# Performance work log

Measured on AMD Instinct MI355X. Metric: run time of the kernel, lower is better.

Reference implementation:

```python
import jax, jax.numpy as jnp
import numpy as np

N_NODES = 100000
N_EDGES = 1600000


def gcn_conv(x, W, b, src, dst, ew, n):
    """PyG GCNConv: x@W, symmetric deg^-1/2 norm with self-loops, scatter-add at dst, +b."""
    loop = jnp.arange(n, dtype=src.dtype)
    s = jnp.concatenate([src, loop])            # sources incl. self-loops
    d = jnp.concatenate([dst, loop])            # targets incl. self-loops
    w = jnp.concatenate([ew, jnp.ones((n,), ew.dtype)])  # self-loop weight = 1
    deg = jax.ops.segment_sum(w, d, num_segments=n)      # weighted in-degree
    dinv = jnp.where(deg > 0, jax.lax.rsqrt(deg), 0.0)
    norm = dinv[s] * w * dinv[d]                # [E+N]
    h = x @ W                                   # [N, F_out]
    msg = h[s] * norm[:, None]                  # gather + per-edge scale
    out = jax.ops.segment_sum(msg, d, num_segments=n)    # scatter-add
    return out + b


def setup_inputs() -> dict:
    key = jax.random.key(0)
    ks = jax.random.split(key, 8)
    in_dim, hid, lat = 128, 128, 64
    x = jax.random.normal(ks[0], (N_NODES, in_dim), jnp.float32)
    edge_index = jax.random.randint(ks[1], (2, N_EDGES), 0, N_NODES, dtype=jnp.int32)
    weights = jax.random.uniform(ks[2], (N_EDGES,), jnp.float32)
    s_in = 1.0 / np.sqrt(in_dim)
    s_h = 1.0 / np.sqrt(hid)
    return {
        "x": x,
        "edge_index": edge_index,
        "weights": weights,
        "W1": jax.random.normal(ks[3], (in_dim, hid), jnp.float32) * s_in,
        "b1": jnp.zeros((hid,), jnp.float32),
        "W2": jax.random.normal(ks[4], (hid, hid), jnp.float32) * s_h,
        "b2": jnp.zeros((hid,), jnp.float32),
        "W_mu": jax.random.normal(ks[5], (hid, lat), jnp.float32) * s_h,
        "b_mu": jnp.zeros((lat,), jnp.float32),
        "W_lv": jax.random.normal(ks[6], (hid, lat), jnp.float32) * s_h,
        "b_lv": jnp.zeros((lat,), jnp.float32),
    }


def reference(x, edge_index, weights, W1, b1, W2, b2, W_mu, b_mu, W_lv, b_lv):
    n = x.shape[0]
    src, dst = edge_index[0], edge_index[1]
    h = jax.nn.relu(gcn_conv(x, W1, b1, src, dst, weights, n))
    h = gcn_conv(h, W2, b2, src, dst, weights, n)
    g = jnp.mean(h, axis=0, keepdims=True)      # [1, hid] global mean pool
    mu = g @ W_mu + b_mu
    logvar = g @ W_lv + b_lv
    return (mu, logvar)
```

## Files before the change

### kernel.cpp

```cpp
#include <hip/hip_runtime.h>


typedef __bf16 bf16x8 __attribute__((ext_vector_type(8)));
typedef float f32x4 __attribute__((ext_vector_type(4)));
typedef float f32x2 __attribute__((ext_vector_type(2)));
typedef unsigned long long u64;

#define RE   2048
#define BSH  8
#define BCAP 5120
#define NBMX 392

__device__ __forceinline__ float bf2f(unsigned short u){
  return __uint_as_float(((unsigned)u) << 16);
}
__device__ __forceinline__ unsigned short f2bf(float f){
  unsigned u = __float_as_uint(f);
  u += 0x7fffu + ((u >> 16) & 1u);
  return (unsigned short)(u >> 16);
}
__device__ __forceinline__ __bf16 us2bf(unsigned short u){
  __bf16 b; __builtin_memcpy(&b, &u, 2); return b;
}
__device__ __forceinline__ float ldf(const void* p, int i, int isf32){
  return isf32 ? ((const float*)p)[i] : bf2f(((const unsigned short*)p)[i]);
}
__device__ __forceinline__ void fma8f8(float* acc, float n, uint2 h){
  f32x2 p0 = __builtin_amdgcn_cvt_pk_f32_fp8((int)h.x, false);
  f32x2 p1 = __builtin_amdgcn_cvt_pk_f32_fp8((int)h.x, true);
  f32x2 p2 = __builtin_amdgcn_cvt_pk_f32_fp8((int)h.y, false);
  f32x2 p3 = __builtin_amdgcn_cvt_pk_f32_fp8((int)h.y, true);
  acc[0] = fmaf(n, p0[0], acc[0]);
  acc[1] = fmaf(n, p0[1], acc[1]);
  acc[2] = fmaf(n, p1[0], acc[2]);
  acc[3] = fmaf(n, p1[1], acc[3]);
  acc[4] = fmaf(n, p2[0], acc[4]);
  acc[5] = fmaf(n, p2[1], acc[5]);
  acc[6] = fmaf(n, p3[0], acc[6]);
  acc[7] = fmaf(n, p3[1], acc[7]);
}

__device__ __forceinline__ void scanBuckets(int* __restrict__ cnt, int* __restrict__ sm,
    int* __restrict__ hrow, int* __restrict__ rrow, int NB, int tid){
  const int K = (NBMX + 255) / 256;
  int c0 = tid * K;
  int loc = 0;
  #pragma unroll
  for (int i = 0; i < K; ++i){
    int j = c0 + i;
    if (j < NB) loc += cnt[j];
  }
  sm[tid] = loc;
  __syncthreads();
  for (int off = 1; off < 256; off <<= 1){
    int tmp = (tid >= off) ? sm[tid - off] : 0;
    __syncthreads();
    sm[tid] += tmp;
    __syncthreads();
  }
  int running = sm[tid] - loc;
  #pragma unroll
  for (int i = 0; i < K; ++i){
    int j = c0 + i;
    if (j < NB){
      int old = cnt[j];
      hrow[j] = old;
      rrow[j] = running;
      cnt[j] = running;
      running += old;
    }
  }
}

__global__ void k_init(const unsigned* __restrict__ xw, int* __restrict__ flag,
                       const void* __restrict__ W1, unsigned short* __restrict__ W1T,
                       float* __restrict__ v){
  __shared__ int s[256];
  int t = threadIdx.x;
  int cnt = 0;
  for (int k = t; k < 4096; k += 256){
    unsigned lo = xw[k] & 0xFFFFu;
    int e = (int)((lo >> 7) & 0xFFu);
    if ((e >= 100 && e <= 141) || (lo & 0x7FFFu) == 0) cnt++;
  }
  s[t] = cnt;
  __syncthreads();
  for (int off = 128; off > 0; off >>= 1){
    if (t < off) s[t] += s[t + off];
    __syncthreads();
  }
  int isf32 = (s[0] < 2458) ? 1 : 0;
  if (blockIdx.x == 0){
    if (t == 0) *flag = isf32;
    if (t < 128) v[t] = 0.0f;
  }
  int gid = blockIdx.x * 256 + t;
  int k = gid & 127, n = gid >> 7;
  W1T[gid] = isf32 ? f2bf(((const float*)W1)[k * 128 + n])
                   : ((const unsigned short*)W1)[k * 128 + n];
}

__global__ void __launch_bounds__(256) k_bin1(const int* __restrict__ src,
    const int* __restrict__ dst, const void* __restrict__ w,
    u64* __restrict__ stagD, u64* __restrict__ stagS,
    int* __restrict__ histD, int* __restrict__ roffD,
    int* __restrict__ histS, int* __restrict__ roffS,
    int E, int NB, const int* __restrict__ flagp){
  __shared__ int cntD[NBMX];
  __shared__ int cntS[NBMX];
  __shared__ u64 stag[RE];
  __shared__ int sm[256];
  int tid = threadIdx.x;
  int r = blockIdx.x;
  for (int i = tid; i < NB; i += 256){ cntD[i] = 0; cntS[i] = 0; }
  __syncthreads();
  int isf32 = *flagp;
  int e0 = r * RE;
  int en = E - e0; if (en > RE) en = RE;
  u64 rec[8];
  #pragma unroll
  for (int k = 0; k < 8; ++k){
    int o = k * 256 + tid;
    rec[k] = ~0ull;
    if (o < en){
      int idx = e0 + o;
      int s_ = src[idx], d_ = dst[idx];
      float wf = ldf(w, idx, isf32);
      int wq = (int)(wf * 32768.0f + 0.5f);
      if (wq > 32767) wq = 32767;
      rec[k] = ((u64)(unsigned)d_ << 32) | ((u64)(unsigned)s_ << 15) | (unsigned)wq;
      atomicAdd(&cntD[d_ >> BSH], 1);
      atomicAdd(&cntS[s_ >> BSH], 1);
    }
  }
  __syncthreads();
  scanBuckets(cntD, sm, histD + (size_t)r * NB, roffD + (size_t)r * NB, NB, tid);
  __syncthreads();
  #pragma unroll
  for (int k = 0; k < 8; ++k){
    if (rec[k] != ~0ull){
      int p = atomicAdd(&cntD[(int)(rec[k] >> 32) >> BSH], 1);
      stag[p] = rec[k];
    }
  }
  __syncthreads();
  u64* opD = stagD + (size_t)r * RE;
  for (int i = tid; i < en; i += 256) opD[i] = stag[i];
  __syncthreads();
  scanBuckets(cntS, sm, histS + (size_t)r * NB, roffS + (size_t)r * NB, NB, tid);
  __syncthreads();
  #pragma unroll
  for (int k = 0; k < 8; ++k){
    if (rec[k] != ~0ull){
      int d_ = (int)(rec[k] >> 32);
      int s_ = (int)((rec[k] >> 15) & 0x1FFFFu);
      unsigned wq = (unsigned)(rec[k] & 32767u);
      u64 rs = ((u64)(unsigned)s_ << 32) | ((u64)(unsigned)d_ << 15) | wq;
      int p = atomicAdd(&cntS[s_ >> BSH], 1);
      stag[p] = rs;
    }
  }
  __syncthreads();
  u64* opS = stagS + (size_t)r * RE;
  for (int i = tid; i < en; i += 256) opS[i] = stag[i];
}

__global__ void __launch_bounds__(256) k_transp(const int* __restrict__ A,
    const int* __restrict__ B, int* __restrict__ AT, int* __restrict__ BT,
    int NR, int NB){
  __shared__ int ta[32][33];
  __shared__ int tb[32][33];
  int bx = (int)blockIdx.x * 32;
  int by = (int)blockIdx.y * 32;
  int tx = threadIdx.x & 31, ty = threadIdx.x >> 5;
  for (int yy = ty; yy < 32; yy += 8){
    int r = by + yy, b = bx + tx;
    int v1 = 0, v2 = 0;
    if (r < NR && b < NB){
      v1 = A[(size_t)r * NB + b];
      v2 = B[(size_t)r * NB + b];
    }
    ta[yy][tx] = v1; tb[yy][tx] = v2;
  }
  __syncthreads();
  for (int yy = ty; yy < 32; yy += 8){
    int b = bx + yy, r = by + tx;
    if (b < NB && r < NR){
      AT[(size_t)b * NR + r] = ta[tx][yy];
      BT[(size_t)b * NR + r] = tb[tx][yy];
    }
  }
}

__global__ void __launch_bounds__(512) k_pass2a(const u64* __restrict__ staging,
    const int* __restrict__ histT, const int* __restrict__ roffT,
    float* __restrict__ dinv, int* __restrict__ cnt, int* __restrict__ rowptr,
    int* __restrict__ bsum, int NR, int N){
  __shared__ unsigned cd[256];
  __shared__ int sm[512];
  int b = blockIdx.x, tid = threadIdx.x;
  int lo = b << BSH;
  int nn = N - lo; if (nn > 256) nn = 256;
  if (tid < 256) cd[tid] = 0u;
  __syncthreads();
  const int* hrow = histT + (size_t)b * NR;
  const int* rrow = roffT + (size_t)b * NR;
  for (int r = tid; r < NR; r += 512){
    int len = hrow[r];
    if (len == 0) continue;
    const u64* rp = staging + (size_t)r * RE + rrow[r];
    for (int k = 0; k < len; ++k){
      u64 rec = rp[k];
      int dl = (int)(rec >> 32) - lo;
      atomicAdd(&cd[dl], (1u << 20) | (unsigned)((rec & 32767u) >> 2));
    }
  }
  __syncthreads();
  int val = 0;
  if (tid < nn){
    unsigned p = cd[tid];
    dinv[lo + tid] = rsqrtf(1.0f + (float)(p & 0xFFFFFu) * (1.0f / 8192.0f));
    cnt[lo + tid] = (int)(p >> 20);
    val = (int)(p >> 20);
  }
  sm[tid] = val;
  __syncthreads();
  for (int off = 1; off < 512; off <<= 1){
    int tmp = (tid >= off) ? sm[tid - off] : 0;
    __syncthreads();
    sm[tid] += tmp;
    __syncthreads();
  }
  if (tid < nn) rowptr[lo + tid] = sm[tid] - val;
  if (tid == 511) bsum[b] = sm[511];
}

__global__ void k_scanB(const int* __restrict__ bsum, int* __restrict__ boffs, int NB){
  __shared__ int s[512];
  int t = threadIdx.x;
  int val = (t < NB) ? bsum[t] : 0;
  s[t] = val;
  __syncthreads();
  for (int off = 1; off < 512; off <<= 1){
    int tmp = (t >= off) ? s[t - off] : 0;
    __syncthreads();
    s[t] += tmp;
    __syncthreads();
  }
  boffs[t] = s[t] - val;
}

__global__ void k_scanC(int* __restrict__ rowptr, const int* __restrict__ boffs, int N){
  int i = blockIdx.x * 256 + threadIdx.x;
  if (i >= N) return;
  rowptr[i] = rowptr[i] + boffs[blockIdx.x];
}

__global__ void __launch_bounds__(512) k_pass2S(const u64* __restrict__ stagS,
    const int* __restrict__ histST, const int* __restrict__ roffST,
    const float* __restrict__ dinv, float* __restrict__ S, int NR, int N){
  __shared__ float SL[256];
  int b = blockIdx.x, tid = threadIdx.x;
  int lo = b << BSH;
  int nn = N - lo; if (nn > 256) nn = 256;
  if (tid < 256) SL[tid] = 0.0f;
  __syncthreads();
  const int* hrow = histST + (size_t)b * NR;
  const int* rrow = roffST + (size_t)b * NR;
  for (int r = tid; r < NR; r += 512){
    int len = hrow[r];
    if (len == 0) continue;
    const u64* rp = stagS + (size_t)r * RE + rrow[r];
    for (int k = 0; k < len; ++k){
      u64 rec = rp[k];
      int s_ = (int)(rec >> 32);
      int d_ = (int)((rec >> 15) & 0x1FFFFu);
      float wqf = (float)(rec & 32767u) * (1.0f / 32768.0f);
      atomicAdd(&SL[s_ - lo], wqf * dinv[d_]);
    }
  }
  __syncthreads();
  if (tid < nn) S[lo + tid] = SL[tid];
}

__global__ void __launch_bounds__(512) k_pass2b(const u64* __restrict__ staging,
    const int* __restrict__ histT, const int* __restrict__ roffT,
    const float* __restrict__ dinv, const int* __restrict__ rowptr,
    const int* __restrict__ cnt, unsigned* __restrict__ edges, int NR, int N){
  __shared__ unsigned recs[BCAP];
  __shared__ int cur[256];
  __shared__ int sb[2];
  int b = blockIdx.x, tid = threadIdx.x;
  int lo = b << BSH;
  int nn = N - lo; if (nn > 256) nn = 256;
  if (tid == 0){
    int base = rowptr[lo];
    sb[0] = base;
    sb[1] = rowptr[lo + nn - 1] + cnt[lo + nn - 1] - base;
  }
  __syncthreads();
  int base = sb[0], tot = sb[1];
  if (tot > BCAP) tot = BCAP;
  if (tid < nn) cur[tid] = rowptr[lo + tid] - base;
  __syncthreads();
  const int* hrow = histT + (size_t)b * NR;
  const int* rrow = roffT + (size_t)b * NR;
  for (int r = tid; r < NR; r += 512){
    int len = hrow[r];
    if (len == 0) continue;
    const u64* rp = staging + (size_t)r * RE + rrow[r];
    for (int k = 0; k < len; ++k){
      u64 rec = rp[k];
      int d_ = (int)(rec >> 32);
      int s_ = (int)((rec >> 15) & 0x1FFFFu);
      int wq = (int)(rec & 32767u);
      float nrm = dinv[s_] * ((float)wq * (1.0f / 32768.0f)) * dinv[d_];
      int nq = (int)(nrm * 32768.0f + 0.5f);
      if (nq > 32767) nq = 32767;
      int p = atomicAdd(&cur[d_ - lo], 1);
      if (p < BCAP) recs[p] = ((unsigned)s_ << 15) | (unsigned)nq;
    }
  }
  __syncthreads();
  unsigned* op = edges + base;
  for (int i = tid; i < tot; i += 512) op[i] = recs[i];
}

__global__ void k_cfacm(const float* __restrict__ S, const float* __restrict__ dinv,
                        const int* __restrict__ rowptr, const int* __restrict__ cnt,
                        float2* __restrict__ dc, int2* __restrict__ rc,
                        unsigned* __restrict__ edges, int E, int N){
  if (blockIdx.x == 0 && threadIdx.x < 16) edges[E + threadIdx.x] = 0u;
  int i = blockIdx.x * 256 + threadIdx.x;
  if (i >= N) return;
  float di = dinv[i];
  dc[i] = make_float2(di * di, di * di + di * S[i]);
  rc[i] = make_int2(rowptr[i], cnt[i]);
}

__global__ void __launch_bounds__(256) k_gemm(const void* __restrict__ xv,
                                              const __bf16* __restrict__ wt,
                                              unsigned char* __restrict__ H, int N,
                                              const int* __restrict__ flagp){
  int wave = (blockIdx.x * blockDim.x + threadIdx.x) >> 6;
  int lane = threadIdx.x & 63;
  int row16 = wave << 4;
  if (row16 >= N) return;
  int isf32 = *flagp;
  int m = lane & 15, q = lane >> 4;
  bf16x8 a0, a1, a2, a3;
  if (isf32){
    const float* ap = (const float*)xv + (size_t)(row16 + m) * 128 + q * 8;
    #pragma unroll
    for (int j = 0; j < 8; ++j){
      a0[j] = us2bf(f2bf(ap[j +  0]));
      a1[j] = us2bf(f2bf(ap[j + 32]));
      a2[j] = us2bf(f2bf(ap[j + 64]));
      a3[j] = us2bf(f2bf(ap[j + 96]));
    }
  } else {
    const __bf16* ap = (const __bf16*)xv + (size_t)(row16 + m) * 128 + q * 8;
    a0 = *(const bf16x8*)(ap +  0);
    a1 = *(const bf16x8*)(ap + 32);
    a2 = *(const bf16x8*)(ap + 64);
    a3 = *(const bf16x8*)(ap + 96);
  }
  for (int nt = 0; nt < 8; ++nt){
    const __bf16* bp = wt + (size_t)(nt * 16 + m) * 128 + q * 8;
    bf16x8 b0 = *(const bf16x8*)(bp +  0);
    bf16x8 b1 = *(const bf16x8*)(bp + 32);
    bf16x8 b2 = *(const bf16x8*)(bp + 64);
    bf16x8 b3 = *(const bf16x8*)(bp + 96);
    f32x4 acc = {0.f, 0.f, 0.f, 0.f};
    acc = __builtin_amdgcn_mfma_f32_16x16x32_bf16(a0, b0, acc, 0, 0, 0);
    acc = __builtin_amdgcn_mfma_f32_16x16x32_bf16(a1, b1, acc, 0, 0, 0);
    acc = __builtin_amdgcn_mfma_f32_16x16x32_bf16(a2, b2, acc, 0, 0, 0);
    acc = __builtin_amdgcn_mfma_f32_16x16x32_bf16(a3, b3, acc, 0, 0, 0);
    unsigned char* op = H + (size_t)(row16 + q * 4) * 128 + nt * 16 + m;
    op[0]   = (unsigned char)(__builtin_amdgcn_cvt_pk_fp8_f32(acc[0], acc[0], 0, false) & 0xFF);
    op[128] = (unsigned char)(__builtin_amdgcn_cvt_pk_fp8_f32(acc[1], acc[1], 0, false) & 0xFF);
    op[256] = (unsigned char)(__builtin_amdgcn_cvt_pk_fp8_f32(acc[2], acc[2], 0, false) & 0xFF);
    op[384] = (unsigned char)(__builtin_amdgcn_cvt_pk_fp8_f32(acc[3], acc[3], 0, false) & 0xFF);
  }
}

__global__ void __launch_bounds__(256) k_agg(const unsigned char* __restrict__ H,
    const int2* __restrict__ rc, const float2* __restrict__ dc,
    const unsigned* __restrict__ edges, const void* __restrict__ b1,
    float* __restrict__ v, int N, int totslots, const int* __restrict__ flagp){
  __shared__ float vsh[128];
  __shared__ float bsh[128];
  int tid = threadIdx.x;
  int isf32 = *flagp;
  if (tid < 128){ vsh[tid] = 0.0f; bsh[tid] = ldf(b1, tid, isf32); }
  __syncthreads();
  int lane = tid & 63;
  int wv = tid >> 6;
  int slot = lane >> 3;
  int q = lane & 7;
  const unsigned char* Hq = H + q * 16;
  float ax[16];
  #pragma unroll
  for (int j = 0; j < 16; ++j) ax[j] = 0.0f;
  int d = ((int)blockIdx.x * 4 + wv) * 8 + slot;
  int2 rcv = make_int2(0, 0); float2 dcv = make_float2(0.f, 0.f);
  uint4 hs = make_uint4(0u, 0u, 0u, 0u);
  if (d < N){
    rcv = rc[d]; dcv = dc[d];
    hs = *(const uint4*)(Hq + (size_t)d * 128);
  }
  while (d < N){
    int dn = d + totslots;
    int2 rcn = make_int2(0, 0); float2 dcn = make_float2(0.f, 0.f);
    uint4 hsn = make_uint4(0u, 0u, 0u, 0u);
    if (dn < N){
      rcn = rc[dn]; dcn = dc[dn];
      hsn = *(const uint4*)(Hq + (size_t)dn * 128);
    }
    float acc[16];
    #pragma unroll
    for (int j = 0; j < 16; ++j) acc[j] = 0.0f;
    fma8f8(acc,     dcv.x, make_uint2(hs.x, hs.y));
    fma8f8(acc + 8, dcv.x, make_uint2(hs.z, hs.w));
    int start = rcv.x, len = rcv.y;
    if (len > 0){
      const unsigned* ep = edges + start;
      unsigned e0 = ep[0], e1 = ep[1], e2 = ep[2], e3 = ep[3];
      uint4 h0 = *(const uint4*)(Hq + (size_t)(e0 >> 15) * 128);
      uint4 h1 = *(const uint4*)(Hq + (size_t)(e1 >> 15) * 128);
      uint4 h2 = *(const uint4*)(Hq + (size_t)(e2 >> 15) * 128);
      #pragma unroll 2
      for (int k = 0; k < len; ++k){
        unsigned en = ep[k + 4];
        uint4 hn = *(const uint4*)(Hq + (size_t)(e3 >> 15) * 128);
        float wn = (float)(e0 & 32767u) * (1.0f / 32768.0f);
        fma8f8(acc,     wn, make_uint2(h0.x, h0.y));
        fma8f8(acc + 8, wn, make_uint2(h0.z, h0.w));
        e0 = e1; e1 = e2; e2 = e3; e3 = en;
        h0 = h1; h1 = h2; h2 = hn;
      }
    }
    #pragma unroll
    for (int j = 0; j < 16; ++j){
      float rj = fmaxf(acc[j] + bsh[q * 16 + j], 0.0f);
      ax[j] = fmaf(dcv.y, rj, ax[j]);
    }
    d = dn; rcv = rcn; dcv = dcn; hs = hsn;
  }
  #pragma unroll
  for (int j = 0; j < 16; ++j){
    ax[j] += __shfl_xor(ax[j], 8);
    ax[j] += __shfl_xor(ax[j], 16);
    ax[j] += __shfl_xor(ax[j], 32);
  }
  if (slot == 0){
    #pragma unroll
    for (int j = 0; j < 16; ++j) atomicAdd(&vsh[q * 16 + j], ax[j]);
  }
  __syncthreads();
  if (tid < 128) atomicAdd(&v[tid], vsh[tid]);
}

__global__ void __launch_bounds__(128) k_head(const float* __restrict__ v,
    const void* __restrict__ W2, const void* __restrict__ b2,
    const void* __restrict__ Wmu, const void* __restrict__ bmu,
    const void* __restrict__ Wlv, const void* __restrict__ blv,
    void* __restrict__ outv, float invN, const int* __restrict__ flagp){
  __shared__ float gsh[128];
  __shared__ float tsh[128];
  int t = threadIdx.x;
  int isf32 = *flagp;
  gsh[t] = v[t] * invN;
  __syncthreads();
  float acc = ldf(b2, t, isf32);
  for (int k = 0; k < 128; ++k) acc = fmaf(gsh[k], ldf(W2, k * 128 + t, isf32), acc);
  tsh[t] = acc;
  __syncthreads();
  int j = t & 63;
  const void* Wp = (t < 64) ? Wmu : Wlv;
  float o = ldf((t < 64) ? bmu : blv, j, isf32);
  for (int k = 0; k < 128; ++k) o = fmaf(tsh[k], ldf(Wp, k * 64 + j, isf32), o);
  if (isf32) ((float*)outv)[t] = o;
  else       ((unsigned short*)outv)[t] = f2bf(o);
}

extern "C" void kernel_launch(void* const* d_in, const int* in_sizes, int n_in,
                              void* d_out, int out_size, void* d_ws, size_t ws_size,
                              hipStream_t stream) {
  const void* x   = d_in[0];
  const int*  ei  = (const int*)d_in[1];
  const void* w   = d_in[2];
  const void* W1  = d_in[3];
  const void* b1  = d_in[4];
  const void* W2  = d_in[5];
  const void* b2  = d_in[6];
  const void* Wmu = d_in[7];
  const void* bmu = d_in[8];
  const void* Wlv = d_in[9];
  const void* blv = d_in[10];

  const int N = in_sizes[0] / 128;
  const int E = in_sizes[2];
  const int* src = ei;
  const int* dst = ei + E;

  char* wsb = (char*)d_ws;
  size_t off = 0;
  auto alloc = [&](size_t bytes) -> void* {
    off = (off + 255) & ~(size_t)255;
    void* p = wsb + off;
    off += bytes;
    return p;
  };
  const int NR  = (E + RE - 1) / RE;
  const int NB  = (N + 255) >> BSH;
  int*   flag     = (int*)  alloc(16);
  float* dinv     = (float*)alloc((size_t)N * 4);
  int*   cnt      = (int*)  alloc((size_t)N * 4);
  int*   rowptr   = (int*)  alloc((size_t)(N + 1) * 4);
  float2* dc      = (float2*)alloc((size_t)N * 8);
  int2*   rc      = (int2*) alloc((size_t)N * 8);
  int*   bsum     = (int*)  alloc(512 * 4);
  int*   boffs    = (int*)  alloc(512 * 4);
  float* v        = (float*)alloc(128 * 4);
  unsigned short* W1T = (unsigned short*)alloc(128 * 128 * 2);
  float* S        = (float*)alloc((size_t)N * 4);
  u64*   stagD    = (u64*)  alloc((size_t)NR * RE * 8);
  u64*   stagS    = (u64*)  alloc((size_t)NR * RE * 8);
  int*   histD    = (int*)  alloc((size_t)NR * NB * 4);
  int*   roffD    = (int*)  alloc((size_t)NR * NB * 4);
  int*   histS    = (int*)  alloc((size_t)NR * NB * 4);
  int*   roffS    = (int*)  alloc((size_t)NR * NB * 4);
  int*   histDT   = (int*)  alloc((size_t)NB * NR * 4);
  int*   roffDT   = (int*)  alloc((size_t)NB * NR * 4);
  int*   histST   = (int*)  alloc((size_t)NB * NR * 4);
  int*   roffST   = (int*)  alloc((size_t)NB * NR * 4);
  unsigned* edges = (unsigned*)alloc((size_t)E * 4 + 64);
  unsigned char* H = (unsigned char*)alloc((size_t)N * 128);
  (void)ws_size; (void)n_in; (void)out_size;

  const int nb_n = (N + 255) / 256;

  k_init<<<64, 256, 0, stream>>>((const unsigned*)x, flag, W1, W1T, v);
  k_bin1<<<NR, 256, 0, stream>>>(src, dst, w, stagD, stagS,
                                 histD, roffD, histS, roffS, E, NB, flag);
  dim3 tg((NB + 31) / 32, (NR + 31) / 32);
  k_transp<<<tg, 256, 0, stream>>>(histD, roffD, histDT, roffDT, NR, NB);
  k_transp<<<tg, 256, 0, stream>>>(histS, roffS, histST, roffST, NR, NB);
  k_pass2a<<<NB, 512, 0, stream>>>(stagD, histDT, roffDT, dinv, cnt, rowptr,
                                   bsum, NR, N);
  k_scanB<<<1, 512, 0, stream>>>(bsum, boffs, NB);
  k_scanC<<<nb_n, 256, 0, stream>>>(rowptr, boffs, N);
  k_pass2S<<<NB, 512, 0, stream>>>(stagS, histST, roffST, dinv, S, NR, N);
  k_pass2b<<<NB, 512, 0, stream>>>(stagD, histDT, roffDT, dinv, rowptr, cnt,
                                   edges, NR, N);
  k_cfacm<<<nb_n, 256, 0, stream>>>(S, dinv, rowptr, cnt, dc, rc, edges, E, N);
  const int nwaves = (N + 15) / 16;
  const int nb_g = (nwaves + 3) / 4;
  k_gemm<<<nb_g, 256, 0, stream>>>(x, (const __bf16*)W1T, H, N, flag);
  const int nb_agg = 1024;
  k_agg<<<nb_agg, 256, 0, stream>>>(H, rc, dc, edges, b1, v, N, nb_agg * 32, flag);
  k_head<<<1, 128, 0, stream>>>(v, W2, b2, Wmu, bmu, Wlv, blv,
                                d_out, 1.0f / (float)N, flag);
}
```

Measured before the change: 328.5 us.

## Merge preprocessing kernels and co-schedule GEMM with edge binning

Folds the X@W1 MFMA GEMM into the edge-binning launch as extra blocks, merges the two histogram transposes into one kernel, and combines the source-sum pass, CSR edge build and per-node coefficient computation into one launch with alternating block roles. The edge padding zeroing moves into the scan kernel. The aim is to cut launch count and let the compute-bound GEMM overlap the memory-bound binning. In exchange, the GEMM blocks now carry the binning kernel's large LDS footprint, which may lower their occupancy.

```diff
diff --git a/kernel.cpp b/kernel.cpp
--- a/kernel.cpp
+++ b/kernel.cpp
@@ -100,17 +100,63 @@
                    : ((const unsigned short*)W1)[k * 128 + n];
 }
 
-__global__ void __launch_bounds__(256) k_bin1(const int* __restrict__ src,
+__global__ void __launch_bounds__(256) k_binG(const int* __restrict__ src,
     const int* __restrict__ dst, const void* __restrict__ w,
     u64* __restrict__ stagD, u64* __restrict__ stagS,
     int* __restrict__ histD, int* __restrict__ roffD,
     int* __restrict__ histS, int* __restrict__ roffS,
-    int E, int NB, const int* __restrict__ flagp){
+    int E, int NB, int NR,
+    const void* __restrict__ xv, const __bf16* __restrict__ wt,
+    unsigned char* __restrict__ H, int N, const int* __restrict__ flagp){
   __shared__ int cntD[NBMX];
   __shared__ int cntS[NBMX];
   __shared__ u64 stag[RE];
   __shared__ int sm[256];
   int tid = threadIdx.x;
+  if ((int)blockIdx.x >= NR){
+    int gb = (int)blockIdx.x - NR;
+    int wave = (gb * 256 + tid) >> 6;
+    int lane = tid & 63;
+    int row16 = wave << 4;
+    if (row16 >= N) return;
+    int isf32 = *flagp;
+    int m = lane & 15, q = lane >> 4;
+    bf16x8 a0, a1, a2, a3;
+    if (isf32){
+      const float* ap = (const float*)xv + (size_t)(row16 + m) * 128 + q * 8;
+      #pragma unroll
+      for (int j = 0; j < 8; ++j){
+        a0[j] = us2bf(f2bf(ap[j +  0]));
+        a1[j] = us2bf(f2bf(ap[j + 32]));
+        a2[j] = us2bf(f2bf(ap[j + 64]));
+        a3[j] = us2bf(f2bf(ap[j + 96]));
+      }
+    } else {
+      const __bf16* ap = (const __bf16*)xv + (size_t)(row16 + m) * 128 + q * 8;
+      a0 = *(const bf16x8*)(ap +  0);
+      a1 = *(const bf16x8*)(ap + 32);
+      a2 = *(const bf16x8*)(ap + 64);
+      a3 = *(const bf16x8*)(ap + 96);
+    }
+    for (int nt = 0; nt < 8; ++nt){
+      const __bf16* bp = wt + (size_t)(nt * 16 + m) * 128 + q * 8;
+      bf16x8 b0 = *(const bf16x8*)(bp +  0);
+      bf16x8 b1 = *(const bf16x8*)(bp + 32);
+      bf16x8 b2 = *(const bf16x8*)(bp + 64);
+      bf16x8 b3 = *(const bf16x8*)(bp + 96);
+      f32x4 acc = {0.f, 0.f, 0.f, 0.f};
+      acc = __builtin_amdgcn_mfma_f32_16x16x32_bf16(a0, b0, acc, 0, 0, 0);
+      acc = __builtin_amdgcn_mfma_f32_16x16x32_bf16(a1, b1, acc, 0, 0, 0);
+      acc = __builtin_amdgcn_mfma_f32_16x16x32_bf16(a2, b2, acc, 0, 0, 0);
+      acc = __builtin_amdgcn_mfma_f32_16x16x32_bf16(a3, b3, acc, 0, 0, 0);
+      unsigned char* op = H + (size_t)(row16 + q * 4) * 128 + nt * 16 + m;
+      op[0]   = (unsigned char)(__builtin_amdgcn_cvt_pk_fp8_f32(acc[0], acc[0], 0, false) & 0xFF);
+      op[128] = (unsigned char)(__builtin_amdgcn_cvt_pk_fp8_f32(acc[1], acc[1], 0, false) & 0xFF);
+      op[256] = (unsigned char)(__builtin_amdgcn_cvt_pk_fp8_f32(acc[2], acc[2], 0, false) & 0xFF);
+      op[384] = (unsigned char)(__builtin_amdgcn_cvt_pk_fp8_f32(acc[3], acc[3], 0, false) & 0xFF);
+    }
+    return;
+  }
   int r = blockIdx.x;
   for (int i = tid; i < NB; i += 256){ cntD[i] = 0; cntS[i] = 0; }
   __syncthreads();
@@ -165,29 +211,33 @@
   for (int i = tid; i < en; i += 256) opS[i] = stag[i];
 }
 
-__global__ void __launch_bounds__(256) k_transp(const int* __restrict__ A,
-    const int* __restrict__ B, int* __restrict__ AT, int* __restrict__ BT,
-    int NR, int NB){
+__global__ void __launch_bounds__(256) k_transp4(const int* __restrict__ A,
+    const int* __restrict__ B, const int* __restrict__ C, const int* __restrict__ D,
+    int* __restrict__ AT, int* __restrict__ BT, int* __restrict__ CT,
+    int* __restrict__ DT, int NR, int NB){
   __shared__ int ta[32][33];
   __shared__ int tb[32][33];
+  __shared__ int tc[32][33];
+  __shared__ int td[32][33];
   int bx = (int)blockIdx.x * 32;
   int by = (int)blockIdx.y * 32;
   int tx = threadIdx.x & 31, ty = threadIdx.x >> 5;
   for (int yy = ty; yy < 32; yy += 8){
     int r = by + yy, b = bx + tx;
-    int v1 = 0, v2 = 0;
+    int v1 = 0, v2 = 0, v3 = 0, v4 = 0;
     if (r < NR && b < NB){
-      v1 = A[(size_t)r * NB + b];
-      v2 = B[(size_t)r * NB + b];
-    }
-    ta[yy][tx] = v1; tb[yy][tx] = v2;
+      size_t o = (size_t)r * NB + b;
+      v1 = A[o]; v2 = B[o]; v3 = C[o]; v4 = D[o];
+    }
+    ta[yy][tx] = v1; tb[yy][tx] = v2; tc[yy][tx] = v3; td[yy][tx] = v4;
   }
   __syncthreads();
   for (int yy = ty; yy < 32; yy += 8){
     int b = bx + yy, r = by + tx;
     if (b < NB && r < NR){
-      AT[(size_t)b * NR + r] = ta[tx][yy];
-      BT[(size_t)b * NR + r] = tb[tx][yy];
+      size_t o = (size_t)b * NR + r;
+      AT[o] = ta[tx][yy]; BT[o] = tb[tx][yy];
+      CT[o] = tc[tx][yy]; DT[o] = td[tx][yy];
     }
   }
 }
@@ -250,49 +300,55 @@
   boffs[t] = s[t] - val;
 }
 
-__global__ void k_scanC(int* __restrict__ rowptr, const int* __restrict__ boffs, int N){
+__global__ void k_scanC(int* __restrict__ rowptr, const int* __restrict__ boffs,
+                        unsigned* __restrict__ edges, int E, int N){
+  if (blockIdx.x == 0 && threadIdx.x >= 240)
+    edges[E + threadIdx.x - 240] = 0u;
   int i = blockIdx.x * 256 + threadIdx.x;
   if (i >= N) return;
   rowptr[i] = rowptr[i] + boffs[blockIdx.x];
 }
 
-__global__ void __launch_bounds__(512) k_pass2S(const u64* __restrict__ stagS,
-    const int* __restrict__ histST, const int* __restrict__ roffST,
-    const float* __restrict__ dinv, float* __restrict__ S, int NR, int N){
-  __shared__ float SL[256];
-  int b = blockIdx.x, tid = threadIdx.x;
-  int lo = b << BSH;
-  int nn = N - lo; if (nn > 256) nn = 256;
-  if (tid < 256) SL[tid] = 0.0f;
-  __syncthreads();
-  const int* hrow = histST + (size_t)b * NR;
-  const int* rrow = roffST + (size_t)b * NR;
-  for (int r = tid; r < NR; r += 512){
-    int len = hrow[r];
-    if (len == 0) continue;
-    const u64* rp = stagS + (size_t)r * RE + rrow[r];
-    for (int k = 0; k < len; ++k){
-      u64 rec = rp[k];
-      int s_ = (int)(rec >> 32);
-      int d_ = (int)((rec >> 15) & 0x1FFFFu);
-      float wqf = (float)(rec & 32767u) * (1.0f / 32768.0f);
-      atomicAdd(&SL[s_ - lo], wqf * dinv[d_]);
-    }
-  }
-  __syncthreads();
-  if (tid < nn) S[lo + tid] = SL[tid];
-}
-
-__global__ void __launch_bounds__(512) k_pass2b(const u64* __restrict__ staging,
-    const int* __restrict__ histT, const int* __restrict__ roffT,
-    const float* __restrict__ dinv, const int* __restrict__ rowptr,
-    const int* __restrict__ cnt, unsigned* __restrict__ edges, int NR, int N){
+__global__ void __launch_bounds__(512) k_post(const u64* __restrict__ stagD,
+    const int* __restrict__ histDT, const int* __restrict__ roffDT,
+    const u64* __restrict__ stagS, const int* __restrict__ histST,
+    const int* __restrict__ roffST, const float* __restrict__ dinv,
+    const int* __restrict__ rowptr, const int* __restrict__ cnt,
+    unsigned* __restrict__ edges, float2* __restrict__ dc, int2* __restrict__ rc,
+    int NR, int N){
   __shared__ unsigned recs[BCAP];
   __shared__ int cur[256];
   __shared__ int sb[2];
-  int b = blockIdx.x, tid = threadIdx.x;
+  int b = (int)blockIdx.x >> 1, tid = threadIdx.x;
   int lo = b << BSH;
   int nn = N - lo; if (nn > 256) nn = 256;
+  if (blockIdx.x & 1){
+    float* SL = (float*)recs;
+    if (tid < 256) SL[tid] = 0.0f;
+    __syncthreads();
+    const int* hrow = histST + (size_t)b * NR;
+    const int* rrow = roffST + (size_t)b * NR;
+    for (int r = tid; r < NR; r += 512){
+      int len = hrow[r];
+      if (len == 0) continue;
+      const u64* rp = stagS + (size_t)r * RE + rrow[r];
+      for (int k = 0; k < len; ++k){
+        u64 rec = rp[k];
+        int s_ = (int)(rec >> 32);
+        int d_ = (int)((rec >> 15) & 0x1FFFFu);
+        float wqf = (float)(rec & 32767u) * (1.0f / 32768.0f);
+        atomicAdd(&SL[s_ - lo], wqf * dinv[d_]);
+      }
+    }
+    __syncthreads();
+    if (tid < nn){
+      int i = lo + tid;
+      float di = dinv[i];
+      dc[i] = make_float2(di * di, di * di + di * SL[tid]);
+      rc[i] = make_int2(rowptr[i], cnt[i]);
+    }
+    return;
+  }
   if (tid == 0){
     int base = rowptr[lo];
     sb[0] = base;
@@ -303,12 +359,12 @@
   if (tot > BCAP) tot = BCAP;
   if (tid < nn) cur[tid] = rowptr[lo + tid] - base;
   __syncthreads();
-  const int* hrow = histT + (size_t)b * NR;
-  const int* rrow = roffT + (size_t)b * NR;
+  const int* hrow = histDT + (size_t)b * NR;
+  const int* rrow = roffDT + (size_t)b * NR;
   for (int r = tid; r < NR; r += 512){
     int len = hrow[r];
     if (len == 0) continue;
-    const u64* rp = staging + (size_t)r * RE + rrow[r];
+    const u64* rp = stagD + (size_t)r * RE + rrow[r];
     for (int k = 0; k < len; ++k){
       u64 rec = rp[k];
       int d_ = (int)(rec >> 32);
@@ -324,64 +380,6 @@
   __syncthreads();
   unsigned* op = edges + base;
   for (int i = tid; i < tot; i += 512) op[i] = recs[i];
-}
-
-__global__ void k_cfacm(const float* __restrict__ S, const float* __restrict__ dinv,
-                        const int* __restrict__ rowptr, const int* __restrict__ cnt,
-                        float2* __restrict__ dc, int2* __restrict__ rc,
-                        unsigned* __restrict__ edges, int E, int N){
-  if (blockIdx.x == 0 && threadIdx.x < 16) edges[E + threadIdx.x] = 0u;
-  int i = blockIdx.x * 256 + threadIdx.x;
-  if (i >= N) return;
-  float di = dinv[i];
-  dc[i] = make_float2(di * di, di * di + di * S[i]);
-  rc[i] = make_int2(rowptr[i], cnt[i]);
-}
-
-__global__ void __launch_bounds__(256) k_gemm(const void* __restrict__ xv,
-                                              const __bf16* __restrict__ wt,
-                                              unsigned char* __restrict__ H, int N,
-                                              const int* __restrict__ flagp){
-  int wave = (blockIdx.x * blockDim.x + threadIdx.x) >> 6;
-  int lane = threadIdx.x & 63;
-  int row16 = wave << 4;
-  if (row16 >= N) return;
-  int isf32 = *flagp;
-  int m = lane & 15, q = lane >> 4;
-  bf16x8 a0, a1, a2, a3;
-  if (isf32){
-    const float* ap = (const float*)xv + (size_t)(row16 + m) * 128 + q * 8;
-    #pragma unroll
-    for (int j = 0; j < 8; ++j){
-      a0[j] = us2bf(f2bf(ap[j +  0]));
-      a1[j] = us2bf(f2bf(ap[j + 32]));
-      a2[j] = us2bf(f2bf(ap[j + 64]));
-      a3[j] = us2bf(f2bf(ap[j + 96]));
-    }
-  } else {
-    const __bf16* ap = (const __bf16*)xv + (size_t)(row16 + m) * 128 + q * 8;
-    a0 = *(const bf16x8*)(ap +  0);
-    a1 = *(const bf16x8*)(ap + 32);
-    a2 = *(const bf16x8*)(ap + 64);
-    a3 = *(const bf16x8*)(ap + 96);
-  }
-  for (int nt = 0; nt < 8; ++nt){
-    const __bf16* bp = wt + (size_t)(nt * 16 + m) * 128 + q * 8;
-    bf16x8 b0 = *(const bf16x8*)(bp +  0);
-    bf16x8 b1 = *(const bf16x8*)(bp + 32);
-    bf16x8 b2 = *(const bf16x8*)(bp + 64);
-    bf16x8 b3 = *(const bf16x8*)(bp + 96);
-    f32x4 acc = {0.f, 0.f, 0.f, 0.f};
-    acc = __builtin_amdgcn_mfma_f32_16x16x32_bf16(a0, b0, acc, 0, 0, 0);
-    acc = __builtin_amdgcn_mfma_f32_16x16x32_bf16(a1, b1, acc, 0, 0, 0);
-    acc = __builtin_amdgcn_mfma_f32_16x16x32_bf16(a2, b2, acc, 0, 0, 0);
-    acc = __builtin_amdgcn_mfma_f32_16x16x32_bf16(a3, b3, acc, 0, 0, 0);
-    unsigned char* op = H + (size_t)(row16 + q * 4) * 128 + nt * 16 + m;
-    op[0]   = (unsigned char)(__builtin_amdgcn_cvt_pk_fp8_f32(acc[0], acc[0], 0, false) & 0xFF);
-    op[128] = (unsigned char)(__builtin_amdgcn_cvt_pk_fp8_f32(acc[1], acc[1], 0, false) & 0xFF);
-    op[256] = (unsigned char)(__builtin_amdgcn_cvt_pk_fp8_f32(acc[2], acc[2], 0, false) & 0xFF);
-    op[384] = (unsigned char)(__builtin_amdgcn_cvt_pk_fp8_f32(acc[3], acc[3], 0, false) & 0xFF);
-  }
 }
 
 __global__ void __launch_bounds__(256) k_agg(const unsigned char* __restrict__ H,
@@ -524,7 +522,6 @@
   int*   boffs    = (int*)  alloc(512 * 4);
   float* v        = (float*)alloc(128 * 4);
   unsigned short* W1T = (unsigned short*)alloc(128 * 128 * 2);
-  float* S        = (float*)alloc((size_t)N * 4);
   u64*   stagD    = (u64*)  alloc((size_t)NR * RE * 8);
   u64*   stagS    = (u64*)  alloc((size_t)NR * RE * 8);
   int*   histD    = (int*)  alloc((size_t)NR * NB * 4);
@@ -540,24 +537,23 @@
   (void)ws_size; (void)n_in; (void)out_size;
 
   const int nb_n = (N + 255) / 256;
+  const int nwaves = (N + 15) / 16;
+  const int nb_g = (nwaves + 3) / 4;
 
   k_init<<<64, 256, 0, stream>>>((const unsigned*)x, flag, W1, W1T, v);
-  k_bin1<<<NR, 256, 0, stream>>>(src, dst, w, stagD, stagS,
-                                 histD, roffD, histS, roffS, E, NB, flag);
+  k_binG<<<NR + nb_g, 256, 0, stream>>>(src, dst, w, stagD, stagS,
+                                        histD, roffD, histS, roffS, E, NB, NR,
+                                        x, (const __bf16*)W1T, H, N, flag);
   dim3 tg((NB + 31) / 32, (NR + 31) / 32);
-  k_transp<<<tg, 256, 0, stream>>>(histD, roffD, histDT, roffDT, NR, NB);
-  k_transp<<<tg, 256, 0, stream>>>(histS, roffS, histST, roffST, NR, NB);
+  k_transp4<<<tg, 256, 0, stream>>>(histD, roffD, histS, roffS,
+                                    histDT, roffDT, histST, roffST, NR, NB);
   k_pass2a<<<NB, 512, 0, stream>>>(stagD, histDT, roffDT, dinv, cnt, rowptr,
                                    bsum, NR, N);
   k_scanB<<<1, 512, 0, stream>>>(bsum, boffs, NB);
-  k_scanC<<<nb_n, 256, 0, stream>>>(rowptr, boffs, N);
-  k_pass2S<<<NB, 512, 0, stream>>>(stagS, histST, roffST, dinv, S, NR, N);
-  k_pass2b<<<NB, 512, 0, stream>>>(stagD, histDT, roffDT, dinv, rowptr, cnt,
-                                   edges, NR, N);
-  k_cfacm<<<nb_n, 256, 0, stream>>>(S, dinv, rowptr, cnt, dc, rc, edges, E, N);
-  const int nwaves = (N + 15) / 16;
-  const int nb_g = (nwaves + 3) / 4;
-  k_gemm<<<nb_g, 256, 0, stream>>>(x, (const __bf16*)W1T, H, N, flag);
+  k_scanC<<<nb_n, 256, 0, stream>>>(rowptr, boffs, edges, E, N);
+  k_post<<<2 * NB, 512, 0, stream>>>(stagD, histDT, roffDT, stagS, histST,
+                                     roffST, dinv, rowptr, cnt, edges, dc, rc,
+                                     NR, N);
   const int nb_agg = 1024;
   k_agg<<<nb_agg, 256, 0, stream>>>(H, rc, dc, edges, b1, v, N, nb_agg * 32, flag);
   k_head<<<1, 128, 0, stream>>>(v, W2, b2, Wmu, bmu, Wlv, blv,
```

Measured after the change: 315.1 us. 1.04x faster.
